# Kernel optimization log

Hardware: AMD Instinct MI355X
Metric: run time of the kernel (lower is better)

The kernel has to match this reference:

```python
import jax, jax.numpy as jnp
import numpy as np

K_DEFAULT = 1000.0  # torch.eye(3).fill_(1000.) fills ALL 9 entries, not just the diagonal
THRESH = 3.0
PENALTY = 10000.0


def setup_inputs() -> dict:
    key = jax.random.key(0)
    k1, k2, k3, k4, k5 = jax.random.split(key, 5)
    N, H, D, C = 2048, 128, 7, 64
    return {
        "start_state": jax.random.normal(k1, (1, D), dtype=jnp.float32),
        "state_batch": jax.random.normal(k2, (N, H, D), dtype=jnp.float32),
        "normals": jax.random.normal(k3, (C, 3), dtype=jnp.float32),
        "jac": jax.random.normal(k4, (C, 3, D), dtype=jnp.float32),
        "forces": jax.random.uniform(k5, (C,), dtype=jnp.float32),
    }


def reference(start_state, state_batch, normals, jac, forces):
    # k_c: torch.eye(3).fill_(1000.) => every entry 1000
    k_c = jnp.full((3, 3), K_DEFAULT, dtype=state_batch.dtype)
    # relative joint state: [N, H, 7]
    sb = state_batch[:, :, :7] - start_state[:, :7]
    # out[c, k] = normals[c, :] @ k_c @ jac[c, :, :]  -> [C, 7]
    out = jnp.einsum('ci,ij,cjk->ck', normals, k_c, jac)
    # deltas[n, h, c] = out[c, :] . sb[n, h, :]  (replaces the double Python loop)
    deltas = jnp.einsum('ck,nhk->nhc', out, sb)
    # fi[n, h] = sum_c (forces[c] + deltas[n, h, c])
    fi = jnp.sum(forces[None, None, :] + deltas, axis=2)
    cost = jnp.where(fi > THRESH, jnp.asarray(PENALTY, fi.dtype), jnp.zeros((), fi.dtype))
    return cost
```

## Files before the change

### kernel.cpp

```cpp
#include <hip/hip_runtime.h>


#define FTC_D 7

__global__ __launch_bounds__(64) void ftc_setup_kernel(
    const float* __restrict__ start_state,
    const float* __restrict__ normals,
    const float* __restrict__ jac,
    const float* __restrict__ forces,
    double* __restrict__ wb)
{
    const int c = threadIdx.x;
    double sn = (double)normals[c * 3 + 0]
              + (double)normals[c * 3 + 1]
              + (double)normals[c * 3 + 2];
    double vals[8];
    #pragma unroll
    for (int k = 0; k < FTC_D; ++k) {
        double tk = (double)jac[c * 21 + 0 * 7 + k]
                  + (double)jac[c * 21 + 1 * 7 + k]
                  + (double)jac[c * 21 + 2 * 7 + k];
        vals[k] = 1000.0 * sn * tk;
    }
    vals[7] = (double)forces[c];

    #pragma unroll
    for (int off = 32; off > 0; off >>= 1) {
        #pragma unroll
        for (int k = 0; k < 8; ++k)
            vals[k] += __shfl_xor(vals[k], off, 64);
    }

    if (c == 0) {
        double b = vals[7];
        #pragma unroll
        for (int k = 0; k < FTC_D; ++k) b -= vals[k] * (double)start_state[k];
        #pragma unroll
        for (int k = 0; k < FTC_D; ++k) wb[k] = vals[k];
        wb[7] = b;
    }
}

__global__ __launch_bounds__(256) void ftc_main_kernel(
    const float* __restrict__ state_batch,
    const double* __restrict__ wb,
    float* __restrict__ out,
    int nquad)
{
    double w0 = wb[0], w1 = wb[1], w2 = wb[2], w3 = wb[3];
    double w4 = wb[4], w5 = wb[5], w6 = wb[6];
    double bias = wb[7];

    int t = blockIdx.x * 256 + threadIdx.x;
    if (t < nquad) {
        const float4* p = (const float4*)(state_batch + (size_t)t * 28);
        float v[28];
        float4* vv = (float4*)v;
        #pragma unroll
        for (int j = 0; j < 7; ++j) vv[j] = p[j];

        float4 o;
        float* ov = &o.x;
        #pragma unroll
        for (int r = 0; r < 4; ++r) {
            const float* s = v + r * 7;
            double fi = bias;
            fi = fma((double)s[0], w0, fi);
            fi = fma((double)s[1], w1, fi);
            fi = fma((double)s[2], w2, fi);
            fi = fma((double)s[3], w3, fi);
            fi = fma((double)s[4], w4, fi);
            fi = fma((double)s[5], w5, fi);
            fi = fma((double)s[6], w6, fi);
            ov[r] = (fi > 3.0) ? 10000.0f : 0.0f;
        }
        ((float4*)out)[t] = o;
    }
}

extern "C" void kernel_launch(void* const* d_in, const int* in_sizes, int n_in,
                              void* d_out, int out_size, void* d_ws, size_t ws_size,
                              hipStream_t stream) {
    const float* start_state = (const float*)d_in[0];
    const float* state_batch = (const float*)d_in[1];
    const float* normals     = (const float*)d_in[2];
    const float* jac         = (const float*)d_in[3];
    const float* forces      = (const float*)d_in[4];
    float* out = (float*)d_out;
    double* wb = (double*)d_ws;

    int ntot  = in_sizes[1] / FTC_D;
    int nquad = ntot / 4;
    int grid  = (nquad + 255) / 256;

    ftc_setup_kernel<<<1, 64, 0, stream>>>(start_state, normals, jac, forces, wb);
    ftc_main_kernel<<<grid, 256, 0, stream>>>(state_batch, wb, out, nquad);
}
```

Before: 68.96 us.

## Fuse setup reduction into main kernel with per-wave redundant weight computation

Merges the single-block setup kernel into the main kernel. Each 64-lane wavefront recomputes the contact-summed weights and bias through shuffles instead of reading them from a workspace. State loads are issued before the reduction so their latency overlaps it. This removes a kernel launch and the serial dependency between the two kernels, at the cost of redundant FP64 reduction work in every wave.

```diff
diff --git a/kernel.cpp b/kernel.cpp
--- a/kernel.cpp
+++ b/kernel.cpp
@@ -3,14 +3,27 @@
 
 #define FTC_D 7
 
-__global__ __launch_bounds__(64) void ftc_setup_kernel(
+__global__ __launch_bounds__(256) void ftc_fused_kernel(
     const float* __restrict__ start_state,
+    const float* __restrict__ state_batch,
     const float* __restrict__ normals,
     const float* __restrict__ jac,
     const float* __restrict__ forces,
-    double* __restrict__ wb)
+    float* __restrict__ out,
+    int nquad)
 {
-    const int c = threadIdx.x;
+    const int t = blockIdx.x * 256 + threadIdx.x;
+    const bool active = (t < nquad);
+
+    float v[28];
+    float4* vv = (float4*)v;
+    if (active) {
+        const float4* p = (const float4*)(state_batch + (size_t)t * 28);
+        #pragma unroll
+        for (int j = 0; j < 7; ++j) vv[j] = p[j];
+    }
+
+    const int c = threadIdx.x & 63;
     double sn = (double)normals[c * 3 + 0]
               + (double)normals[c * 3 + 1]
               + (double)normals[c * 3 + 2];
@@ -31,47 +44,25 @@
             vals[k] += __shfl_xor(vals[k], off, 64);
     }
 
-    if (c == 0) {
-        double b = vals[7];
-        #pragma unroll
-        for (int k = 0; k < FTC_D; ++k) b -= vals[k] * (double)start_state[k];
-        #pragma unroll
-        for (int k = 0; k < FTC_D; ++k) wb[k] = vals[k];
-        wb[7] = b;
-    }
-}
+    double bias = vals[7];
+    #pragma unroll
+    for (int k = 0; k < FTC_D; ++k)
+        bias -= vals[k] * (double)start_state[k];
 
-__global__ __launch_bounds__(256) void ftc_main_kernel(
-    const float* __restrict__ state_batch,
-    const double* __restrict__ wb,
-    float* __restrict__ out,
-    int nquad)
-{
-    double w0 = wb[0], w1 = wb[1], w2 = wb[2], w3 = wb[3];
-    double w4 = wb[4], w5 = wb[5], w6 = wb[6];
-    double bias = wb[7];
-
-    int t = blockIdx.x * 256 + threadIdx.x;
-    if (t < nquad) {
-        const float4* p = (const float4*)(state_batch + (size_t)t * 28);
-        float v[28];
-        float4* vv = (float4*)v;
-        #pragma unroll
-        for (int j = 0; j < 7; ++j) vv[j] = p[j];
-
+    if (active) {
         float4 o;
         float* ov = &o.x;
         #pragma unroll
         for (int r = 0; r < 4; ++r) {
             const float* s = v + r * 7;
             double fi = bias;
-            fi = fma((double)s[0], w0, fi);
-            fi = fma((double)s[1], w1, fi);
-            fi = fma((double)s[2], w2, fi);
-            fi = fma((double)s[3], w3, fi);
-            fi = fma((double)s[4], w4, fi);
-            fi = fma((double)s[5], w5, fi);
-            fi = fma((double)s[6], w6, fi);
+            fi = fma((double)s[0], vals[0], fi);
+            fi = fma((double)s[1], vals[1], fi);
+            fi = fma((double)s[2], vals[2], fi);
+            fi = fma((double)s[3], vals[3], fi);
+            fi = fma((double)s[4], vals[4], fi);
+            fi = fma((double)s[5], vals[5], fi);
+            fi = fma((double)s[6], vals[6], fi);
             ov[r] = (fi > 3.0) ? 10000.0f : 0.0f;
         }
         ((float4*)out)[t] = o;
@@ -87,12 +78,11 @@
     const float* jac         = (const float*)d_in[3];
     const float* forces      = (const float*)d_in[4];
     float* out = (float*)d_out;
-    double* wb = (double*)d_ws;
 
     int ntot  = in_sizes[1] / FTC_D;
     int nquad = ntot / 4;
     int grid  = (nquad + 255) / 256;
 
-    ftc_setup_kernel<<<1, 64, 0, stream>>>(start_state, normals, jac, forces, wb);
-    ftc_main_kernel<<<grid, 256, 0, stream>>>(state_batch, wb, out, nquad);
+    ftc_fused_kernel<<<grid, 256, 0, stream>>>(
+        start_state, state_batch, normals, jac, forces, out, nquad);
 }
```

Result: no change. 68.11 us (-1.2%).
